# Kernel tuning notes

Hardware: AMD Instinct MI355X
Metric: run time of the kernel (lower is better)

Reference implementation:

```python
import jax, jax.numpy as jnp
import numpy as np

N = 50000      # nodes
E = 600000     # edges
D = 128        # dim_h == num_features
G = 512        # graphs in batch
BN_EPS = 1e-5


def _w(k, shape, fan_in):
    return jax.random.normal(k, shape, jnp.float32) * np.float32(1.0 / np.sqrt(fan_in))


def setup_inputs() -> dict:
    key = jax.random.key(0)
    ks = jax.random.split(key, 16)
    return {
        "x": jax.random.normal(ks[0], (N, D), jnp.float32),
        "edge_index": jax.random.randint(ks[1], (2, E), 0, N, jnp.int64),
        "batch": jnp.sort(jax.random.randint(ks[2], (N,), 0, G, jnp.int64)),
        # GINConv 1 MLP: Linear -> BN -> ReLU -> Linear -> ReLU
        "c1_W1": _w(ks[3], (D, D), D), "c1_b1": jnp.zeros((D,), jnp.float32),
        "c1_g": jnp.ones((D,), jnp.float32), "c1_be": jnp.zeros((D,), jnp.float32),
        "c1_W2": _w(ks[4], (D, D), D), "c1_b2": jnp.zeros((D,), jnp.float32),
        # GINConv 2 MLP
        "c2_W1": _w(ks[5], (D, D), D), "c2_b1": jnp.zeros((D,), jnp.float32),
        "c2_g": jnp.ones((D,), jnp.float32), "c2_be": jnp.zeros((D,), jnp.float32),
        "c2_W2": _w(ks[6], (D, D), D), "c2_b2": jnp.zeros((D,), jnp.float32),
        # readout MLP
        "lin1_W": _w(ks[7], (4 * D, 4 * D), 4 * D), "lin1_b": jnp.zeros((4 * D,), jnp.float32),
        "lin2_W": _w(ks[8], (4 * D, 1), 4 * D), "lin2_b": jnp.zeros((1,), jnp.float32),
    }


def _gin_conv(x, src, dst, W1, b1, g, be, W2, b2):
    # sum aggregation of neighbor messages (PyG GINConv, eps=0)
    agg = jax.ops.segment_sum(x[src], dst, num_segments=x.shape[0])
    h = (agg + x) @ W1 + b1
    # BatchNorm1d, training mode (biased batch stats over nodes)
    mu = h.mean(axis=0)
    var = h.var(axis=0)
    h = jax.nn.relu(g * (h - mu) * jax.lax.rsqrt(var + BN_EPS) + be)
    return jax.nn.relu(h @ W2 + b2)


def _pool(h, batch):
    add = jax.ops.segment_sum(h, batch, num_segments=G)
    mx = jax.ops.segment_max(h, batch, num_segments=G)
    mx = jnp.where(jnp.isfinite(mx), mx, 0.0)  # empty segments -> 0
    return add, mx


def reference(x, edge_index, batch,
              c1_W1, c1_b1, c1_g, c1_be, c1_W2, c1_b2,
              c2_W1, c2_b1, c2_g, c2_be, c2_W2, c2_b2,
              lin1_W, lin1_b, lin2_W, lin2_b):
    src, dst = edge_index[0], edge_index[1]
    h1 = _gin_conv(x, src, dst, c1_W1, c1_b1, c1_g, c1_be, c1_W2, c1_b2)
    h2 = _gin_conv(h1, src, dst, c2_W1, c2_b1, c2_g, c2_be, c2_W2, c2_b2)
    a1, m1 = _pool(h1, batch)
    a2, m2 = _pool(h2, batch)
    h = jnp.concatenate([a1, a2, m1, m2], axis=1)  # [G, 4D]
    h = jax.nn.relu(h @ lin1_W + lin1_b)
    h = h @ lin2_W + lin2_b  # [G, 1]
    return jax.nn.sigmoid(h), h
```

## Files before the change

### kernel.cpp

```cpp
#include <hip/hip_runtime.h>

#define D 128
#define GNUM 512

typedef _Float16 f16;
typedef _Float16 f16x8 __attribute__((ext_vector_type(8)));
typedef float f32x4 __attribute__((ext_vector_type(4)));

__global__ void deg_kernel(const int* __restrict__ ei, int* __restrict__ deg,
                           int nE) {
  int e = blockIdx.x * blockDim.x + threadIdx.x;
  if (e < nE) atomicAdd(&deg[ei[nE + e]], 1);
}

__global__ __launch_bounds__(256) void partial_kernel(
    const int* __restrict__ deg, int* __restrict__ partials, int n) {
  __shared__ int sh[256];
  const int t = threadIdx.x;
  const int i = blockIdx.x * 512 + t * 2;
  int s = 0;
  if (i < n) s += deg[i];
  if (i + 1 < n) s += deg[i + 1];
  sh[t] = s;
  __syncthreads();
#pragma unroll
  for (int off = 128; off > 0; off >>= 1) {
    if (t < off) sh[t] += sh[t + off];
    __syncthreads();
  }
  if (t == 0) partials[blockIdx.x] = sh[0];
}

__global__ __launch_bounds__(128) void scanp_kernel(
    int* __restrict__ partials, int nP, int* __restrict__ rowptr, int n,
    int nE) {
  __shared__ int sh[128];
  const int t = threadIdx.x;
  const int v = (t < nP) ? partials[t] : 0;
  sh[t] = v;
  __syncthreads();
#pragma unroll
  for (int off = 1; off < 128; off <<= 1) {
    int u = (t >= off) ? sh[t - off] : 0;
    __syncthreads();
    sh[t] += u;
    __syncthreads();
  }
  if (t < nP) partials[t] = sh[t] - v;
  if (t == 0) rowptr[n] = nE;
}

__global__ __launch_bounds__(256) void emit_kernel(
    const int* __restrict__ deg, const int* __restrict__ partials,
    int* __restrict__ rowptr, int* __restrict__ cursor, int n) {
  __shared__ int sh[256];
  const int t = threadIdx.x;
  const int i = blockIdx.x * 512 + t * 2;
  const int d0 = (i < n) ? deg[i] : 0;
  const int d1 = (i + 1 < n) ? deg[i + 1] : 0;
  const int s = d0 + d1;
  sh[t] = s;
  __syncthreads();
#pragma unroll
  for (int off = 1; off < 256; off <<= 1) {
    int u = (t >= off) ? sh[t - off] : 0;
    __syncthreads();
    sh[t] += u;
    __syncthreads();
  }
  int base = partials[blockIdx.x] + sh[t] - s;
  if (i < n) {
    rowptr[i] = base;
    cursor[i] = base;
    base += d0;
  }
  if (i + 1 < n) {
    rowptr[i + 1] = base;
    cursor[i + 1] = base;
  }
}

__global__ void fill_kernel(const int* __restrict__ ei, int* __restrict__ cursor,
                            int* __restrict__ csr, int nE) {
  int e = blockIdx.x * blockDim.x + threadIdx.x;
  if (e < nE) {
    int d = ei[nE + e];
    int pos = atomicAdd(&cursor[d], 1);
    csr[pos] = ei[e];
  }
}

__global__ void gstart_kernel(const int* __restrict__ batch,
                              int* __restrict__ gstart, int n) {
  int g = blockIdx.x * blockDim.x + threadIdx.x;
  if (g > GNUM) return;
  if (g == GNUM) { gstart[g] = n; return; }
  int lo = 0, hi = n;
  while (lo < hi) {
    int mid = (lo + hi) >> 1;
    if (batch[mid] < g) lo = mid + 1; else hi = mid;
  }
  gstart[g] = lo;
}

__global__ void xcvt_kernel(const float* __restrict__ in, f16* __restrict__ out,
                            int n4) {
  int i = blockIdx.x * 256 + threadIdx.x;
  if (i < n4) {
    float4 v = ((const float4*)in)[i];
    union { f16 h[4]; uint2 u; } p;
    p.h[0] = (f16)v.x; p.h[1] = (f16)v.y; p.h[2] = (f16)v.z; p.h[3] = (f16)v.w;
    ((uint2*)out)[i] = p.u;
  }
}

__global__ void wprep_kernel(const float* __restrict__ W0,
                             const float* __restrict__ W1,
                             const float* __restrict__ W2,
                             const float* __restrict__ W3,
                             f16* __restrict__ out) {
  int idx = blockIdx.x * 256 + threadIdx.x;
  int wsel = idx >> 14;
  int rem = idx & 16383;
  int col = rem >> 7, k = rem & 127;
  const float* W = (wsel == 0) ? W0 : (wsel == 1) ? W1 : (wsel == 2) ? W2 : W3;
  out[idx] = (f16)W[k * D + col];
}

__global__ __launch_bounds__(256) void agg16_kernel(
    const f16* __restrict__ feat, const int* __restrict__ rowptr,
    const int* __restrict__ csr, f16* __restrict__ out, int n) {
  int row = blockIdx.x * 16 + (threadIdx.x >> 4);
  int q = threadIdx.x & 15;
  if (row >= n) return;
  const int co = q * 8;
  float a[8];
  f16x8 v = *(const f16x8*)(feat + (size_t)row * D + co);
#pragma unroll
  for (int j = 0; j < 8; j++) a[j] = (float)v[j];
  int beg = rowptr[row], end = rowptr[row + 1];
  int i = beg;
  for (; i + 1 < end; i += 2) {
    int s0 = csr[i], s1 = csr[i + 1];
    f16x8 v0 = *(const f16x8*)(feat + (size_t)s0 * D + co);
    f16x8 v1 = *(const f16x8*)(feat + (size_t)s1 * D + co);
#pragma unroll
    for (int j = 0; j < 8; j++) a[j] += (float)v0[j] + (float)v1[j];
  }
  if (i < end) {
    f16x8 v0 = *(const f16x8*)(feat + (size_t)csr[i] * D + co);
#pragma unroll
    for (int j = 0; j < 8; j++) a[j] += (float)v0[j];
  }
  f16x8 o;
#pragma unroll
  for (int j = 0; j < 8; j++) o[j] = (f16)a[j];
  *(f16x8*)(out + (size_t)row * D + co) = o;
}

template <int BN, int OUT>
__global__ __launch_bounds__(64) void gemm16_kernel(
    const f16* __restrict__ A, const float* __restrict__ ss,
    const f16* __restrict__ WT, const float* __restrict__ bias,
    f16* __restrict__ C, float* __restrict__ pstat, int n) {
  const int l = threadIdx.x;
  const int rw0 = blockIdx.x * 32;
  const int lr = l & 15;
  const int lq = l >> 4;
  const int lk = lq * 8;

  f32x4 acc[2][8];
#pragma unroll
  for (int m = 0; m < 2; m++)
#pragma unroll
    for (int nt = 0; nt < 8; nt++) acc[m][nt] = (f32x4)0.f;

#pragma unroll
  for (int s = 0; s < 4; s++) {
    const int k = s * 32 + lk;
    f16x8 af[2];
#pragma unroll
    for (int m = 0; m < 2; m++) {
      int row = rw0 + m * 16 + lr;
      f16x8 v = (f16x8)(f16)0.f;
      if (row < n) v = *(const f16x8*)(A + (size_t)row * D + k);
      if (BN) {
        float4 c0 = *(const float4*)(ss + k);
        float4 c1 = *(const float4*)(ss + k + 4);
        float4 h0 = *(const float4*)(ss + 128 + k);
        float4 h1 = *(const float4*)(ss + 128 + k + 4);
        f16x8 r;
        r[0] = (f16)fmaxf(0.f, fmaf((float)v[0], c0.x, h0.x));
        r[1] = (f16)fmaxf(0.f, fmaf((float)v[1], c0.y, h0.y));
        r[2] = (f16)fmaxf(0.f, fmaf((float)v[2], c0.z, h0.z));
        r[3] = (f16)fmaxf(0.f, fmaf((float)v[3], c0.w, h0.w));
        r[4] = (f16)fmaxf(0.f, fmaf((float)v[4], c1.x, h1.x));
        r[5] = (f16)fmaxf(0.f, fmaf((float)v[5], c1.y, h1.y));
        r[6] = (f16)fmaxf(0.f, fmaf((float)v[6], c1.z, h1.z));
        r[7] = (f16)fmaxf(0.f, fmaf((float)v[7], c1.w, h1.w));
        af[m] = r;
      } else {
        af[m] = v;
      }
    }
    f16x8 bf[8];
#pragma unroll
    for (int nt = 0; nt < 8; nt++) {
      int col = nt * 16 + lr;
      bf[nt] = *(const f16x8*)(WT + (size_t)col * D + k);
    }
#pragma unroll
    for (int m = 0; m < 2; m++)
#pragma unroll
      for (int nt = 0; nt < 8; nt++)
        acc[m][nt] = __builtin_amdgcn_mfma_f32_16x16x32_f16(af[m], bf[nt],
                                                            acc[m][nt], 0, 0, 0);
  }

  if constexpr (OUT == 0) {
    float ts[8], tq[8];
#pragma unroll
    for (int nt = 0; nt < 8; nt++) { ts[nt] = 0.f; tq[nt] = 0.f; }
#pragma unroll
    for (int m = 0; m < 2; m++)
#pragma unroll
      for (int r = 0; r < 4; r++) {
        int row = rw0 + m * 16 + lq * 4 + r;
        if (row < n) {
#pragma unroll
          for (int nt = 0; nt < 8; nt++) {
            float v = acc[m][nt][r] + bias[nt * 16 + lr];
            C[(size_t)row * D + nt * 16 + lr] = (f16)v;
            ts[nt] += v;
            tq[nt] = fmaf(v, v, tq[nt]);
          }
        }
      }
#pragma unroll
    for (int nt = 0; nt < 8; nt++) {
      ts[nt] += __shfl_xor(ts[nt], 16); ts[nt] += __shfl_xor(ts[nt], 32);
      tq[nt] += __shfl_xor(tq[nt], 16); tq[nt] += __shfl_xor(tq[nt], 32);
    }
    if (l < 16) {
      float* ps = pstat + (size_t)blockIdx.x * 256;
#pragma unroll
      for (int nt = 0; nt < 8; nt++) {
        ps[nt * 16 + l] = ts[nt];
        ps[128 + nt * 16 + l] = tq[nt];
      }
    }
  } else {
#pragma unroll
    for (int m = 0; m < 2; m++)
#pragma unroll
      for (int r = 0; r < 4; r++) {
        int row = rw0 + m * 16 + lq * 4 + r;
        if (row < n) {
#pragma unroll
          for (int nt = 0; nt < 8; nt++) {
            float v = fmaxf(0.f, acc[m][nt][r] + bias[nt * 16 + lr]);
            C[(size_t)row * D + nt * 16 + lr] = (f16)v;
          }
        }
      }
  }
}

__global__ __launch_bounds__(256) void statreduce_kernel(
    const float* __restrict__ pstat, float* __restrict__ colsum, int nB) {
  int c = threadIdx.x;
  float s = 0.f;
  for (int b = blockIdx.x; b < nB; b += gridDim.x)
    s += pstat[(size_t)b * 256 + c];
  atomicAdd(colsum + c, s);
}

__global__ void bnstats_kernel(const float* __restrict__ colsum,
                               const float* __restrict__ g,
                               const float* __restrict__ be,
                               float* __restrict__ ss, int n) {
  int c = threadIdx.x;
  float inv_n = 1.0f / (float)n;
  float mean = colsum[c] * inv_n;
  float var = colsum[128 + c] * inv_n - mean * mean;
  float scale = g[c] * rsqrtf(var + 1e-5f);
  ss[c] = scale;
  ss[128 + c] = be[c] - mean * scale;
}

__global__ __launch_bounds__(256) void pool2_kernel(
    const f16* __restrict__ h1, const f16* __restrict__ h2,
    const int* __restrict__ gstart, float* __restrict__ pooled) {
  int g = blockIdx.x;
  int c = threadIdx.x & 127;
  int half = threadIdx.x >> 7;
  int r0 = gstart[g], r1 = gstart[g + 1];
  float s1 = 0.f, m1 = 0.f, s2 = 0.f, m2 = 0.f;
  for (int r = r0 + half; r < r1; r += 2) {
    float v1 = (float)h1[(size_t)r * D + c];
    float v2 = (float)h2[(size_t)r * D + c];
    s1 += v1; m1 = fmaxf(m1, v1);
    s2 += v2; m2 = fmaxf(m2, v2);
  }
  __shared__ float sh[256];
  sh[threadIdx.x] = s1; __syncthreads();
  if (half == 0) s1 += sh[threadIdx.x + 128];
  __syncthreads(); sh[threadIdx.x] = s2; __syncthreads();
  if (half == 0) s2 += sh[threadIdx.x + 128];
  __syncthreads(); sh[threadIdx.x] = m1; __syncthreads();
  if (half == 0) m1 = fmaxf(m1, sh[threadIdx.x + 128]);
  __syncthreads(); sh[threadIdx.x] = m2; __syncthreads();
  if (half == 0) {
    m2 = fmaxf(m2, sh[threadIdx.x + 128]);
    float* pg = pooled + (size_t)g * 512;
    pg[c] = s1;
    pg[128 + c] = s2;
    pg[256 + c] = m1;
    pg[384 + c] = m2;
  }
}

__global__ __launch_bounds__(512) void lin1_kernel(
    const float* __restrict__ pooled, const float* __restrict__ W,
    float* __restrict__ out1) {
  __shared__ float prow[4][128];
  const int j = threadIdx.x;
  const int gt = blockIdx.x >> 2;
  const int kt = blockIdx.x & 3;
  const int g0 = gt * 4, k0 = kt * 128;
  prow[j >> 7][j & 127] = pooled[(size_t)(g0 + (j >> 7)) * 512 + k0 + (j & 127)];
  __syncthreads();
  float acc[4] = {0.f, 0.f, 0.f, 0.f};
  for (int k = 0; k < 128; k++) {
    float w = W[(size_t)(k0 + k) * 512 + j];
#pragma unroll
    for (int r = 0; r < 4; r++) acc[r] = fmaf(prow[r][k], w, acc[r]);
  }
#pragma unroll
  for (int r = 0; r < 4; r++)
    atomicAdd(out1 + (size_t)(g0 + r) * 512 + j, acc[r]);
}

__global__ void lin2_kernel(const float* __restrict__ out1,
                            const float* __restrict__ b1,
                            const float* __restrict__ W,
                            const float* __restrict__ b2,
                            float* __restrict__ out) {
  int g = blockIdx.x;
  int lane = threadIdx.x;
  float s = 0.f;
  for (int k = lane; k < 512; k += 64)
    s = fmaf(fmaxf(0.f, out1[(size_t)g * 512 + k] + b1[k]), W[k], s);
#pragma unroll
  for (int off = 32; off > 0; off >>= 1) s += __shfl_down(s, off);
  if (lane == 0) {
    float h = s + b2[0];
    out[g] = 1.0f / (1.0f + expf(-h));
    out[GNUM + g] = h;
  }
}

extern "C" void kernel_launch(void* const* d_in, const int* in_sizes, int n_in,
                              void* d_out, int out_size, void* d_ws,
                              size_t ws_size, hipStream_t stream) {
  const float* x = (const float*)d_in[0];
  const int* ei = (const int*)d_in[1];
  const int* batch = (const int*)d_in[2];
  const float* c1_W1 = (const float*)d_in[3];
  const float* c1_b1 = (const float*)d_in[4];
  const float* c1_g  = (const float*)d_in[5];
  const float* c1_be = (const float*)d_in[6];
  const float* c1_W2 = (const float*)d_in[7];
  const float* c1_b2 = (const float*)d_in[8];
  const float* c2_W1 = (const float*)d_in[9];
  const float* c2_b1 = (const float*)d_in[10];
  const float* c2_g  = (const float*)d_in[11];
  const float* c2_be = (const float*)d_in[12];
  const float* c2_W2 = (const float*)d_in[13];
  const float* c2_b2 = (const float*)d_in[14];
  const float* lin1_W = (const float*)d_in[15];
  const float* lin1_b = (const float*)d_in[16];
  const float* lin2_W = (const float*)d_in[17];
  const float* lin2_b = (const float*)d_in[18];

  const int n = in_sizes[0] / D;
  const int nE = in_sizes[1] / 2;

  char* p = (char*)d_ws;
  auto take = [&](size_t bytes) {
    char* r = p;
    p += (bytes + 255) & ~(size_t)255;
    return r;
  };
  f16*   hpre   = (f16*)take((size_t)n * D * 2);
  f16*   aggt   = (f16*)take((size_t)n * D * 2);
  f16*   h1     = (f16*)take((size_t)n * D * 2);
  f16*   wt     = (f16*)take(4 * 16384 * 2);
  float* pooled = (float*)take((size_t)GNUM * 512 * 4);
  float* out1b  = (float*)take((size_t)GNUM * 512 * 4);
  float* colsum = (float*)take(256 * 4);
  int*   gstart = (int*)take((GNUM + 1) * 4);
  int* deg      = (int*)take((size_t)n * 4);
  int* rowptr   = (int*)take((size_t)(n + 1) * 4);
  int* cursor   = (int*)take((size_t)(n + 1) * 4);
  int* partials = (int*)take(128 * 4);
  int* csr      = (int*)take((size_t)nE * 4);
  const int nB = (n + 31) / 32;
  float* pstat  = (float*)take((size_t)nB * 256 * 4);

  const int edge_grid = (nE + 255) / 256;
  const int agg_grid = (n + 15) / 16;
  const int nP = (n + 511) / 512;
  const int n4 = n * D / 4;

  hipMemsetAsync(deg, 0, (size_t)n * sizeof(int), stream);
  hipMemsetAsync(out1b, 0, (size_t)GNUM * 512 * sizeof(float), stream);
  deg_kernel<<<edge_grid, 256, 0, stream>>>(ei, deg, nE);
  partial_kernel<<<nP, 256, 0, stream>>>(deg, partials, n);
  scanp_kernel<<<1, 128, 0, stream>>>(partials, nP, rowptr, n, nE);
  emit_kernel<<<nP, 256, 0, stream>>>(deg, partials, rowptr, cursor, n);
  fill_kernel<<<edge_grid, 256, 0, stream>>>(ei, cursor, csr, nE);
  gstart_kernel<<<3, 256, 0, stream>>>(batch, gstart, n);
  wprep_kernel<<<256, 256, 0, stream>>>(c1_W1, c1_W2, c2_W1, c2_W2, wt);
  xcvt_kernel<<<(n4 + 255) / 256, 256, 0, stream>>>(x, h1, n4);

  agg16_kernel<<<agg_grid, 256, 0, stream>>>(h1, rowptr, csr, aggt, n);
  gemm16_kernel<0, 0><<<nB, 64, 0, stream>>>(aggt, nullptr, wt, c1_b1, hpre,
                                             pstat, n);
  hipMemsetAsync(colsum, 0, 256 * sizeof(float), stream);
  statreduce_kernel<<<32, 256, 0, stream>>>(pstat, colsum, nB);
  bnstats_kernel<<<1, 128, 0, stream>>>(colsum, c1_g, c1_be, colsum, n);
  gemm16_kernel<1, 1><<<nB, 64, 0, stream>>>(hpre, colsum, wt + 16384, c1_b2,
                                             h1, nullptr, n);

  agg16_kernel<<<agg_grid, 256, 0, stream>>>(h1, rowptr, csr, aggt, n);
  gemm16_kernel<0, 0><<<nB, 64, 0, stream>>>(aggt, nullptr, wt + 32768, c2_b1,
                                             hpre, pstat, n);
  hipMemsetAsync(colsum, 0, 256 * sizeof(float), stream);
  statreduce_kernel<<<32, 256, 0, stream>>>(pstat, colsum, nB);
  bnstats_kernel<<<1, 128, 0, stream>>>(colsum, c2_g, c2_be, colsum, n);
  gemm16_kernel<1, 1><<<nB, 64, 0, stream>>>(hpre, colsum, wt + 49152, c2_b2,
                                             aggt, nullptr, n);

  pool2_kernel<<<GNUM, 256, 0, stream>>>(h1, aggt, gstart, pooled);
  lin1_kernel<<<512, 512, 0, stream>>>(pooled, lin1_W, out1b);
  lin2_kernel<<<GNUM, 64, 0, stream>>>(out1b, lin1_b, lin2_W, lin2_b,
                                       (float*)d_out);
}
```

Before: 279.2 us.

## Aggregate with one wavefront per row, drop colsum atomics and memsets

The neighbor aggregation now gives each node row a full 64-lane wavefront, with each lane reading 2 halves per neighbor and four neighbors unrolled per iteration. Before, 16 lanes each read 8 halves, so every gather is now one 256-byte coalesced read per wave and there is more memory parallelism per row. The BN statistics reduction now writes per-block partials that bnstats sums itself, which removes the atomicAdd and the colsum memsets. The deg buffer is also placed next to out1b so a single memset clears both. In exchange, each lane issues narrower 4-byte loads and more waves are launched.

```diff
diff --git a/kernel.cpp b/kernel.cpp
--- a/kernel.cpp
+++ b/kernel.cpp
@@ -4,6 +4,7 @@
 #define GNUM 512
 
 typedef _Float16 f16;
+typedef _Float16 f16x2 __attribute__((ext_vector_type(2)));
 typedef _Float16 f16x8 __attribute__((ext_vector_type(8)));
 typedef float f32x4 __attribute__((ext_vector_type(4)));
 
@@ -127,35 +128,38 @@
   out[idx] = (f16)W[k * D + col];
 }
 
-__global__ __launch_bounds__(256) void agg16_kernel(
+__global__ __launch_bounds__(256) void aggw_kernel(
     const f16* __restrict__ feat, const int* __restrict__ rowptr,
     const int* __restrict__ csr, f16* __restrict__ out, int n) {
-  int row = blockIdx.x * 16 + (threadIdx.x >> 4);
-  int q = threadIdx.x & 15;
+  const int row = blockIdx.x * 4 + (threadIdx.x >> 6);
+  const int l = threadIdx.x & 63;
   if (row >= n) return;
-  const int co = q * 8;
-  float a[8];
-  f16x8 v = *(const f16x8*)(feat + (size_t)row * D + co);
-#pragma unroll
-  for (int j = 0; j < 8; j++) a[j] = (float)v[j];
-  int beg = rowptr[row], end = rowptr[row + 1];
+  const int c = l * 2;
+  float a0, a1;
+  {
+    f16x2 v = *(const f16x2*)(feat + (size_t)row * D + c);
+    a0 = (float)v[0]; a1 = (float)v[1];
+  }
+  const int beg = rowptr[row], end = rowptr[row + 1];
   int i = beg;
-  for (; i + 1 < end; i += 2) {
-    int s0 = csr[i], s1 = csr[i + 1];
-    f16x8 v0 = *(const f16x8*)(feat + (size_t)s0 * D + co);
-    f16x8 v1 = *(const f16x8*)(feat + (size_t)s1 * D + co);
-#pragma unroll
-    for (int j = 0; j < 8; j++) a[j] += (float)v0[j] + (float)v1[j];
-  }
-  if (i < end) {
-    f16x8 v0 = *(const f16x8*)(feat + (size_t)csr[i] * D + co);
-#pragma unroll
-    for (int j = 0; j < 8; j++) a[j] += (float)v0[j];
-  }
-  f16x8 o;
-#pragma unroll
-  for (int j = 0; j < 8; j++) o[j] = (f16)a[j];
-  *(f16x8*)(out + (size_t)row * D + co) = o;
+  for (; i + 3 < end; i += 4) {
+    int s0 = csr[i], s1 = csr[i + 1], s2 = csr[i + 2], s3 = csr[i + 3];
+    f16x2 v0 = *(const f16x2*)(feat + (size_t)s0 * D + c);
+    f16x2 v1 = *(const f16x2*)(feat + (size_t)s1 * D + c);
+    f16x2 v2 = *(const f16x2*)(feat + (size_t)s2 * D + c);
+    f16x2 v3 = *(const f16x2*)(feat + (size_t)s3 * D + c);
+    a0 += (float)v0[0] + (float)v1[0] + (float)v2[0] + (float)v3[0];
+    a1 += (float)v0[1] + (float)v1[1] + (float)v2[1] + (float)v3[1];
+  }
+  for (; i < end; i++) {
+    f16x2 v = *(const f16x2*)(feat + (size_t)csr[i] * D + c);
+    a0 += (float)v[0];
+    a1 += (float)v[1];
+  }
+  f16x2 o;
+  o[0] = (f16)a0;
+  o[1] = (f16)a1;
+  *(f16x2*)(out + (size_t)row * D + c) = o;
 }
 
 template <int BN, int OUT>
@@ -205,10 +209,8 @@
     }
     f16x8 bf[8];
 #pragma unroll
-    for (int nt = 0; nt < 8; nt++) {
-      int col = nt * 16 + lr;
-      bf[nt] = *(const f16x8*)(WT + (size_t)col * D + k);
-    }
+    for (int nt = 0; nt < 8; nt++)
+      bf[nt] = *(const f16x8*)(WT + (size_t)(nt * 16 + lr) * D + k);
 #pragma unroll
     for (int m = 0; m < 2; m++)
 #pragma unroll
@@ -267,22 +269,28 @@
 }
 
 __global__ __launch_bounds__(256) void statreduce_kernel(
-    const float* __restrict__ pstat, float* __restrict__ colsum, int nB) {
+    const float* __restrict__ pstat, float* __restrict__ pstat2, int nB) {
   int c = threadIdx.x;
   float s = 0.f;
-  for (int b = blockIdx.x; b < nB; b += gridDim.x)
+  for (int b = blockIdx.x; b < nB; b += 32)
     s += pstat[(size_t)b * 256 + c];
-  atomicAdd(colsum + c, s);
-}
-
-__global__ void bnstats_kernel(const float* __restrict__ colsum,
+  pstat2[(size_t)blockIdx.x * 256 + c] = s;
+}
+
+__global__ void bnstats_kernel(const float* __restrict__ pstat2,
                                const float* __restrict__ g,
                                const float* __restrict__ be,
                                float* __restrict__ ss, int n) {
   int c = threadIdx.x;
+  float s = 0.f, sq = 0.f;
+#pragma unroll
+  for (int i = 0; i < 32; i++) {
+    s += pstat2[i * 256 + c];
+    sq += pstat2[i * 256 + 128 + c];
+  }
   float inv_n = 1.0f / (float)n;
-  float mean = colsum[c] * inv_n;
-  float var = colsum[128 + c] * inv_n - mean * mean;
+  float mean = s * inv_n;
+  float var = sq * inv_n - mean * mean;
   float scale = g[c] * rsqrtf(var + 1e-5f);
   ss[c] = scale;
   ss[128 + c] = be[c] - mean * scale;
@@ -398,23 +406,23 @@
   f16*   wt     = (f16*)take(4 * 16384 * 2);
   float* pooled = (float*)take((size_t)GNUM * 512 * 4);
   float* out1b  = (float*)take((size_t)GNUM * 512 * 4);
-  float* colsum = (float*)take(256 * 4);
+  int*   deg    = (int*)take((size_t)n * 4);
+  float* ssbuf  = (float*)take(256 * 4);
   int*   gstart = (int*)take((GNUM + 1) * 4);
-  int* deg      = (int*)take((size_t)n * 4);
   int* rowptr   = (int*)take((size_t)(n + 1) * 4);
   int* cursor   = (int*)take((size_t)(n + 1) * 4);
   int* partials = (int*)take(128 * 4);
   int* csr      = (int*)take((size_t)nE * 4);
   const int nB = (n + 31) / 32;
   float* pstat  = (float*)take((size_t)nB * 256 * 4);
+  float* pstat2 = (float*)take(32 * 256 * 4);
 
   const int edge_grid = (nE + 255) / 256;
-  const int agg_grid = (n + 15) / 16;
+  const int aggw_grid = (n + 3) / 4;
   const int nP = (n + 511) / 512;
   const int n4 = n * D / 4;
 
-  hipMemsetAsync(deg, 0, (size_t)n * sizeof(int), stream);
-  hipMemsetAsync(out1b, 0, (size_t)GNUM * 512 * sizeof(float), stream);
+  hipMemsetAsync(out1b, 0, (size_t)GNUM * 512 * 4 + (size_t)n * 4, stream);
   deg_kernel<<<edge_grid, 256, 0, stream>>>(ei, deg, nE);
   partial_kernel<<<nP, 256, 0, stream>>>(deg, partials, n);
   scanp_kernel<<<1, 128, 0, stream>>>(partials, nP, rowptr, n, nE);
@@ -424,22 +432,20 @@
   wprep_kernel<<<256, 256, 0, stream>>>(c1_W1, c1_W2, c2_W1, c2_W2, wt);
   xcvt_kernel<<<(n4 + 255) / 256, 256, 0, stream>>>(x, h1, n4);
 
-  agg16_kernel<<<agg_grid, 256, 0, stream>>>(h1, rowptr, csr, aggt, n);
+  aggw_kernel<<<aggw_grid, 256, 0, stream>>>(h1, rowptr, csr, aggt, n);
   gemm16_kernel<0, 0><<<nB, 64, 0, stream>>>(aggt, nullptr, wt, c1_b1, hpre,
                                              pstat, n);
-  hipMemsetAsync(colsum, 0, 256 * sizeof(float), stream);
-  statreduce_kernel<<<32, 256, 0, stream>>>(pstat, colsum, nB);
-  bnstats_kernel<<<1, 128, 0, stream>>>(colsum, c1_g, c1_be, colsum, n);
-  gemm16_kernel<1, 1><<<nB, 64, 0, stream>>>(hpre, colsum, wt + 16384, c1_b2,
+  statreduce_kernel<<<32, 256, 0, stream>>>(pstat, pstat2, nB);
+  bnstats_kernel<<<1, 128, 0, stream>>>(pstat2, c1_g, c1_be, ssbuf, n);
+  gemm16_kernel<1, 1><<<nB, 64, 0, stream>>>(hpre, ssbuf, wt + 16384, c1_b2,
                                              h1, nullptr, n);
 
-  agg16_kernel<<<agg_grid, 256, 0, stream>>>(h1, rowptr, csr, aggt, n);
+  aggw_kernel<<<aggw_grid, 256, 0, stream>>>(h1, rowptr, csr, aggt, n);
   gemm16_kernel<0, 0><<<nB, 64, 0, stream>>>(aggt, nullptr, wt + 32768, c2_b1,
                                              hpre, pstat, n);
-  hipMemsetAsync(colsum, 0, 256 * sizeof(float), stream);
-  statreduce_kernel<<<32, 256, 0, stream>>>(pstat, colsum, nB);
-  bnstats_kernel<<<1, 128, 0, stream>>>(colsum, c2_g, c2_be, colsum, n);
-  gemm16_kernel<1, 1><<<nB, 64, 0, stream>>>(hpre, colsum, wt + 49152, c2_b2,
+  statreduce_kernel<<<32, 256, 0, stream>>>(pstat, pstat2, nB);
+  bnstats_kernel<<<1, 128, 0, stream>>>(pstat2, c2_g, c2_be, ssbuf, n);
+  gemm16_kernel<1, 1><<<nB, 64, 0, stream>>>(hpre, ssbuf, wt + 49152, c2_b2,
                                              aggt, nullptr, n);
 
   pool2_kernel<<<GNUM, 256, 0, stream>>>(h1, aggt, gstart, pooled);
```

New measurement: 282.8 us. About the same (+1.3%).
